# Kernel optimization log

Hardware: AMD Instinct MI355X
Metric: run time of the kernel (lower is better)

The kernel has to match this reference:

```python
import jax, jax.numpy as jnp
import numpy as np

B, N, D, H, NCB, TOPK = 4, 2048, 256, 2048, 256, 16
DP = D // 4
SCALE = float(np.sqrt(DP))
THRESH = 0.7
EPS = 1e-8


def setup_inputs() -> dict:
    key = jax.random.key(0)
    ks = jax.random.split(key, 12)
    g = lambda i, shape, s=1.0: jax.random.normal(ks[i], shape, jnp.float32) * s
    return {
        "agent_states": g(0, (B, N, D)),
        "agent_actions": g(1, (B, N, D)),
        "episodic_mem": g(2, (B, N, H)),
        "Wq": g(3, (D, DP), 0.05), "bq": jnp.zeros((DP,), jnp.float32),
        "Wk": g(4, (D, DP), 0.05), "bk": jnp.zeros((DP,), jnp.float32),
        "log_temp": jnp.asarray(0.0, jnp.float32),
        "Wc": g(5, (D, DP), 0.05), "bc": jnp.zeros((DP,), jnp.float32),
        "temp_coal": jnp.asarray(10.0, jnp.float32),
        "W_to_hdc": g(6, (D, H), 0.05), "b_to_hdc": jnp.zeros((H,), jnp.float32),
        "W_from_hdc": g(7, (H, D), 0.02), "b_from_hdc": jnp.zeros((D,), jnp.float32),
        "agent_keys": jnp.sign(g(8, (N, H))),
        "position_codes": jnp.sign(g(9, (NCB, H))),
        "step": 3,
    }


def _cosine(a, b):
    # torch F.cosine_similarity semantics, dim=-1, eps=1e-8
    na = jnp.maximum(jnp.linalg.norm(a, axis=-1), EPS)
    nb = jnp.maximum(jnp.linalg.norm(b, axis=-1), EPS)
    return jnp.sum(a * b, axis=-1) / (na * nb)


def _to_hdc_ste(x):
    soft = jnp.tanh(x * 3.0)
    hard = jnp.sign(x)
    hard = jnp.where(hard == 0, jnp.ones_like(hard), hard)
    return soft + jax.lax.stop_gradient(hard - soft)


def reference(agent_states, agent_actions, episodic_mem, Wq, bq, Wk, bk,
              log_temp, Wc, bc, temp_coal, W_to_hdc, b_to_hdc,
              W_from_hdc, b_from_hdc, agent_keys, position_codes, step):
    # ---- DynamicGraph.compute_graph: top-k dynamic attention adjacency ----
    Q = agent_actions @ Wq + bq                      # (B,N,DP)
    K = agent_actions @ Wk + bk                      # (B,N,DP)
    temp = jnp.clip(jnp.exp(log_temp), 0.1, 10.0)
    scores = jnp.einsum('bnd,bmd->bnm', Q, K) / (SCALE * temp)   # (B,N,N)
    _, topk_idx = jax.lax.top_k(scores, TOPK)                     # (B,N,k)
    bI = jnp.arange(B)[:, None, None]
    nI = jnp.arange(N)[None, :, None]
    mask = jnp.zeros_like(scores).at[bI, nI, topk_idx].set(1.0)   # scatter, like torch scatter_
    scores = scores * mask + (1.0 - mask) * -1e9
    adjacency = jax.nn.softmax(scores, axis=-1)
    # message passing over dynamic graph
    incoming = jnp.einsum('bnm,bmd->bnd', adjacency, agent_states)

    # ---- AgentCombination: sigmoid-normalized coalition mixing ----
    proj = agent_actions @ Wc + bc                   # (B,N,DP)
    pn = proj / jnp.maximum(jnp.linalg.norm(proj, axis=-1, keepdims=True), 1e-12)
    sim = jnp.einsum('bnd,bmd->bnm', pn, pn)
    cw = jax.nn.sigmoid((sim - THRESH) * temp_coal)
    cw = cw / (jnp.sum(cw, axis=-1, keepdims=True) + EPS)
    combined = jnp.einsum('bnm,bmd->bnd', cw, incoming)
    mixed = 0.8 * incoming + 0.2 * combined          # (B,N,D)

    # ---- HDCMemory: bind / write / read with STE ----
    q = _to_hdc_ste(mixed @ W_to_hdc + b_to_hdc)     # (B,N,H) bipolar via STE
    pq = q * agent_keys[None]                        # bind with agent key
    mem = jax.lax.stop_gradient(episodic_mem)        # memory read is detached in original
    pos_code = position_codes[step % NCB]            # (H,)
    new_mem = 0.95 * mem + 0.05 * (q * pos_code)     # write: bind + decay bundle
    strength = jax.nn.sigmoid(_cosine(new_mem, pq))[..., None]   # read similarity
    recall = (new_mem @ W_from_hdc + b_from_hdc) * strength      # (B,N,D)
    return mixed + recall
```

## Files before the change

kernel.cpp:

```cpp
#include <hip/hip_runtime.h>
#include <math.h>

#define BATCH 4
#define NN 2048
#define DD 256
#define HH 2048
#define DP 64
#define KTOP 16

typedef float f32x4 __attribute__((ext_vector_type(4)));
typedef short short8 __attribute__((ext_vector_type(8)));
typedef short short4v __attribute__((ext_vector_type(4)));

__device__ __forceinline__ short f2bf(float x) {
    union { float f; unsigned u; } v; v.f = x;
    unsigned r = v.u + 0x7FFFu + ((v.u >> 16) & 1u);
    return (short)(r >> 16);
}
__device__ __forceinline__ float bf2f(short s) {
    union { unsigned u; float f; } v; v.u = ((unsigned)(unsigned short)s) << 16;
    return v.f;
}

__global__ __launch_bounds__(256) void head_kernel(
    const float* __restrict__ act,
    const float* __restrict__ Wq, const float* __restrict__ bq,
    const float* __restrict__ Wk, const float* __restrict__ bk,
    const float* __restrict__ Wc, const float* __restrict__ bc,
    const float* __restrict__ W2h, const float* __restrict__ Wfh,
    float* __restrict__ Qo, float* __restrict__ Ko, short* __restrict__ Pno,
    short* __restrict__ W2hT_hi, short* __restrict__ W2hT_lo,
    short* __restrict__ WfhT_hi, short* __restrict__ WfhT_lo)
{
    __shared__ float smem[16 * 256];

    if (blockIdx.x < 512) {
        float (*rowbuf)[256] = (float(*)[256])smem;
        const int row0 = blockIdx.x * 16;
        const int t = threadIdx.x;
        const int wave = t >> 6, lane = t & 63;
        const float* src = act + (size_t)row0 * DD;
        for (int i = t; i < 16 * DD; i += 256) rowbuf[i >> 8][i & 255] = src[i];
        __syncthreads();

        float q[4], k[4], c[4];
        #pragma unroll
        for (int r = 0; r < 4; ++r) { q[r] = bq[lane]; k[r] = bk[lane]; c[r] = bc[lane]; }

        for (int d = 0; d < DD; ++d) {
            float wq = Wq[d * DP + lane];
            float wk = Wk[d * DP + lane];
            float wc = Wc[d * DP + lane];
            #pragma unroll
            for (int r = 0; r < 4; ++r) {
                float av = rowbuf[wave * 4 + r][d];
                q[r] = fmaf(av, wq, q[r]);
                k[r] = fmaf(av, wk, k[r]);
                c[r] = fmaf(av, wc, c[r]);
            }
        }
        #pragma unroll
        for (int r = 0; r < 4; ++r) {
            float ss = c[r] * c[r];
            #pragma unroll
            for (int off = 32; off; off >>= 1) ss += __shfl_xor(ss, off);
            float nrm = fmaxf(sqrtf(ss), 1e-12f);
            size_t o = (size_t)(row0 + wave * 4 + r) * DP + lane;
            Qo[o] = q[r];
            Ko[o] = k[r];
            Pno[o] = f2bf(c[r] / nrm);
        }
    } else {
        float (*tile)[33] = (float(*)[33])smem;
        int b = blockIdx.x - 512;
        const float* src; short *dhi, *dlo; int R, C, r0, c0;
        if (b < 512) {
            src = W2h; dhi = W2hT_hi; dlo = W2hT_lo; R = 256; C = 2048;
            r0 = (b >> 6) * 32; c0 = (b & 63) * 32;
        } else {
            b -= 512;
            src = Wfh; dhi = WfhT_hi; dlo = WfhT_lo; R = 2048; C = 256;
            r0 = (b >> 3) * 32; c0 = (b & 7) * 32;
        }
        int tx = threadIdx.x & 31, ty = threadIdx.x >> 5;
        #pragma unroll
        for (int i = 0; i < 4; ++i)
            tile[ty + 8 * i][tx] = src[(size_t)(r0 + ty + 8 * i) * C + c0 + tx];
        __syncthreads();
        #pragma unroll
        for (int i = 0; i < 4; ++i) {
            float v = tile[tx][ty + 8 * i];
            short hi = f2bf(v);
            size_t o = (size_t)(c0 + ty + 8 * i) * R + r0 + tx;
            dhi[o] = hi;
            dlo[o] = f2bf(v - bf2f(hi));
        }
    }
}

__global__ __launch_bounds__(512, 4) void attn_fused_kernel(
    const float* __restrict__ Q, const float* __restrict__ K,
    const float* __restrict__ log_temp,
    const float* __restrict__ states, float* __restrict__ incoming)
{
    const int t = threadIdx.x;
    const int w = t >> 6, l = t & 63;
    const int row = blockIdx.x * 8 + w;
    const int b = row >> 11;

    __shared__ float Ksh[128][68];

    const float temp = fminf(fmaxf(expf(log_temp[0]), 0.1f), 10.0f);
    const float scale = 1.0f / (8.0f * temp);

    const float* Kb = K + (size_t)b * NN * DP;
    const float4* qr4 = (const float4*)(Q + (size_t)row * DP);

    float sc[32];

    for (int ch = 0; ch < 16; ++ch) {
        __syncthreads();
        {
            int r = t >> 2, seg = t & 3;
            const float4* src = (const float4*)(Kb + (size_t)(ch * 128 + r) * DP + seg * 16);
            float4* dst = (float4*)&Ksh[r][seg * 16];
            dst[0] = src[0]; dst[1] = src[1]; dst[2] = src[2]; dst[3] = src[3];
        }
        __syncthreads();
        float a0 = 0.f, a1 = 0.f;
        const float4* k0 = (const float4*)&Ksh[l][0];
        const float4* k1 = (const float4*)&Ksh[64 + l][0];
        #pragma unroll
        for (int h = 0; h < 2; ++h) {
            float4 q[8];
            #pragma unroll
            for (int i = 0; i < 8; ++i) q[i] = qr4[h * 8 + i];
            #pragma unroll
            for (int i = 0; i < 8; ++i) {
                float4 kv0 = k0[h * 8 + i];
                float4 kv1 = k1[h * 8 + i];
                a0 = fmaf(kv0.x, q[i].x, fmaf(kv0.y, q[i].y, fmaf(kv0.z, q[i].z, fmaf(kv0.w, q[i].w, a0))));
                a1 = fmaf(kv1.x, q[i].x, fmaf(kv1.y, q[i].y, fmaf(kv1.z, q[i].z, fmaf(kv1.w, q[i].w, a1))));
            }
        }
        sc[ch * 2]     = a0 * scale;
        sc[ch * 2 + 1] = a1 * scale;
    }

    float wv = 0.f; int wm = 0;
    for (int it = 0; it < KTOP; ++it) {
        float bv = sc[0]; int bs = 0;
        #pragma unroll
        for (int i = 1; i < 32; ++i) {
            bool g = sc[i] > bv;
            bv = g ? sc[i] : bv;
            bs = g ? i : bs;
        }
        int bm = (bs >> 1) * 128 + (bs & 1) * 64 + l;
        #pragma unroll
        for (int off = 1; off < 64; off <<= 1) {
            float ov = __shfl_xor(bv, off);
            int   om = __shfl_xor(bm, off);
            bool take = (ov > bv) || (ov == bv && om < bm);
            bv = take ? ov : bv;
            bm = take ? om : bm;
        }
        if (l == it) { wv = bv; wm = bm; }
        if ((bm & 63) == l) {
            int s = ((bm >> 7) << 1) | ((bm >> 6) & 1);
            #pragma unroll
            for (int i = 0; i < 32; ++i) if (s == i) sc[i] = -3.0e38f;
        }
    }

    float mx = __shfl(wv, 0);
    float e = (l < KTOP) ? expf(wv - mx) : 0.f;
    float Z = e;
    #pragma unroll
    for (int off = 1; off < 64; off <<= 1) Z += __shfl_xor(Z, off);
    float wnorm = e / Z;

    const float* Sb = states + (size_t)b * NN * DD;
    f32x4 acc = (f32x4){0.f, 0.f, 0.f, 0.f};
    #pragma unroll
    for (int kk = 0; kk < KTOP; ++kk) {
        float wk = __shfl(wnorm, kk);
        int   ik = __shfl(wm, kk);
        const float4 v = *(const float4*)(Sb + (size_t)ik * DD + l * 4);
        acc[0] = fmaf(wk, v.x, acc[0]);
        acc[1] = fmaf(wk, v.y, acc[1]);
        acc[2] = fmaf(wk, v.z, acc[2]);
        acc[3] = fmaf(wk, v.w, acc[3]);
    }
    *(float4*)(incoming + (size_t)row * DD + l * 4) = *(float4*)&acc;
}

__global__ __launch_bounds__(256) void coal_kernel(
    const short* __restrict__ pnb_g, const float* __restrict__ incoming,
    const float* __restrict__ temp_coal, float* __restrict__ mixed)
{
    const int b  = blockIdx.x >> 7;
    const int rem = blockIdx.x & 127;
    const int n0 = (rem >> 1) * 32;
    const int dh = rem & 1;
    const int t = threadIdx.x;
    const int w = t >> 6;
    const int l = t & 63;

    __shared__ alignas(16) short pnA[32][72];
    __shared__ alignas(16) short pnB[64][72];
    __shared__ alignas(16) short cwt[32][72];
    __shared__ alignas(16) short incT[128][72];
    __shared__ float rowsum[32];

    const size_t bbase = (size_t)b * NN;

    {
        int r = t >> 3, k8 = (t & 7) * 8;
        *(short8*)&pnA[r][k8] = *(const short8*)(pnb_g + (bbase + n0 + r) * DP + k8);
    }
    if (t < 32) rowsum[t] = 0.0f;

    const float tc = temp_coal[0];

    f32x4 acc[2][2];
    #pragma unroll
    for (int i = 0; i < 2; ++i)
        #pragma unroll
        for (int j = 0; j < 2; ++j)
            acc[i][j] = (f32x4){0.f, 0.f, 0.f, 0.f};

    const int lrow = l & 15;
    const int lk   = (l >> 4) * 8;

    for (int ch = 0; ch < 32; ++ch) {
        const int m0 = ch * 64;
        __syncthreads();

        {
            int r = t >> 2, kq = (t & 3) * 16;
            const short* src = pnb_g + (bbase + m0 + r) * DP + kq;
            *(short8*)&pnB[r][kq]     = *(const short8*)src;
            *(short8*)&pnB[r][kq + 8] = *(const short8*)(src + 8);
        }
        {
            #pragma unroll
            for (int rep = 0; rep < 2; ++rep) {
                int id = t + rep * 256;
                int mq = id & 15;
                int dq = id >> 4;
                const float* incb = incoming + (bbase + m0 + mq * 4) * DD + dh * 128 + dq * 4;
                short4v col0, col1, col2, col3;
                #pragma unroll
                for (int mm = 0; mm < 4; ++mm) {
                    float4 v = *(const float4*)(incb + (size_t)mm * DD);
                    col0[mm] = f2bf(v.x);
                    col1[mm] = f2bf(v.y);
                    col2[mm] = f2bf(v.z);
                    col3[mm] = f2bf(v.w);
                }
                *(short4v*)&incT[dq * 4 + 0][mq * 4] = col0;
                *(short4v*)&incT[dq * 4 + 1][mq * 4] = col1;
                *(short4v*)&incT[dq * 4 + 2][mq * 4] = col2;
                *(short4v*)&incT[dq * 4 + 3][mq * 4] = col3;
            }
        }
        __syncthreads();

        f32x4 sacc[2];
        sacc[0] = (f32x4){0.f, 0.f, 0.f, 0.f};
        sacc[1] = (f32x4){0.f, 0.f, 0.f, 0.f};
        #pragma unroll
        for (int ks = 0; ks < 2; ++ks) {
            short8 bfr = *(const short8*)&pnB[w * 16 + lrow][lk + ks * 32];
            short8 a0  = *(const short8*)&pnA[lrow][lk + ks * 32];
            short8 a1  = *(const short8*)&pnA[16 + lrow][lk + ks * 32];
            sacc[0] = __builtin_amdgcn_mfma_f32_16x16x32_bf16(a0, bfr, sacc[0], 0, 0, 0);
            sacc[1] = __builtin_amdgcn_mfma_f32_16x16x32_bf16(a1, bfr, sacc[1], 0, 0, 0);
        }
        #pragma unroll
        for (int rt = 0; rt < 2; ++rt) {
            #pragma unroll
            for (int j = 0; j < 4; ++j) {
                int rr = rt * 16 + (l >> 4) * 4 + j;
                int cc = w * 16 + lrow;
                float cv = 1.0f / (1.0f + expf(-(sacc[rt][j] - 0.7f) * tc));
                cwt[rr][cc] = f2bf(cv);
            }
        }
        __syncthreads();

        {
            int r = t >> 3, c8 = (t & 7) * 8;
            short8 cv = *(const short8*)&cwt[r][c8];
            float p = 0.f;
            #pragma unroll
            for (int j = 0; j < 8; ++j) p += bf2f(cv[j]);
            p += __shfl_xor(p, 1);
            p += __shfl_xor(p, 2);
            p += __shfl_xor(p, 4);
            if ((t & 7) == 0) rowsum[r] += p;
        }

        #pragma unroll
        for (int ks = 0; ks < 2; ++ks) {
            short8 a0 = *(const short8*)&cwt[lrow][lk + ks * 32];
            short8 a1 = *(const short8*)&cwt[16 + lrow][lk + ks * 32];
            #pragma unroll
            for (int ct = 0; ct < 2; ++ct) {
                short8 bfr = *(const short8*)&incT[w * 32 + ct * 16 + lrow][lk + ks * 32];
                acc[0][ct] = __builtin_amdgcn_mfma_f32_16x16x32_bf16(a0, bfr, acc[0][ct], 0, 0, 0);
                acc[1][ct] = __builtin_amdgcn_mfma_f32_16x16x32_bf16(a1, bfr, acc[1][ct], 0, 0, 0);
            }
        }
    }
    __syncthreads();

    #pragma unroll
    for (int rt = 0; rt < 2; ++rt) {
        #pragma unroll
        for (int ct = 0; ct < 2; ++ct) {
            #pragma unroll
            for (int j = 0; j < 4; ++j) {
                int rr = rt * 16 + (l >> 4) * 4 + j;
                int cc = w * 32 + ct * 16 + lrow;
                float inv = 1.0f / (rowsum[rr] + 1e-8f);
                float comb = acc[rt][ct][j] * inv;
                size_t gi = (bbase + n0 + rr) * DD + dh * 128 + cc;
                mixed[gi] = 0.8f * incoming[gi] + 0.2f * comb;
            }
        }
    }
}

__global__ __launch_bounds__(256) void hdcA_kernel(
    const float* __restrict__ mixed,
    const short* __restrict__ W2hT_hi, const short* __restrict__ W2hT_lo,
    const float* __restrict__ b2h,
    unsigned short* __restrict__ qbits)
{
    const int rb = blockIdx.x >> 3;
    const int hs = blockIdx.x & 7;
    const int row0 = rb * 32;
    const int hbase = hs * 256;
    const int t = threadIdx.x;
    const int w = t >> 6, l = t & 63;
    const int lr = l & 15, lg = l >> 4;

    __shared__ short Ahi[32][264], Alo[32][264];
    __shared__ short Whi[64][136], Wlo[64][136];

    #pragma unroll
    for (int i = 0; i < 8; ++i) {
        int idx = t + i * 256;
        int r = idx >> 6, c = (idx & 63) * 4;
        float4 v = *(const float4*)(mixed + (size_t)(row0 + r) * DD + c);
        short4v hi4, lo4;
        hi4[0] = f2bf(v.x); lo4[0] = f2bf(v.x - bf2f(hi4[0]));
        hi4[1] = f2bf(v.y); lo4[1] = f2bf(v.y - bf2f(hi4[1]));
        hi4[2] = f2bf(v.z); lo4[2] = f2bf(v.z - bf2f(hi4[2]));
        hi4[3] = f2bf(v.w); lo4[3] = f2bf(v.w - bf2f(hi4[3]));
        *(short4v*)&Ahi[r][c] = hi4;
        *(short4v*)&Alo[r][c] = lo4;
    }

    for (int ch = 0; ch < 4; ++ch) {
        const int h0 = hbase + ch * 64;
        f32x4 zac[2];
        zac[0] = (f32x4){0.f, 0.f, 0.f, 0.f};
        zac[1] = (f32x4){0.f, 0.f, 0.f, 0.f};
        #pragma unroll
        for (int ks = 0; ks < 2; ++ks) {
            const int k0 = ks * 128;
            __syncthreads();
            {
                int r = t >> 2, cb = (t & 3) * 32;
                const short* sh = W2hT_hi + (size_t)(h0 + r) * DD + k0 + cb;
                const short* sl = W2hT_lo + (size_t)(h0 + r) * DD + k0 + cb;
                #pragma unroll
                for (int j = 0; j < 4; ++j) {
                    *(short8*)&Whi[r][cb + j * 8] = *(const short8*)(sh + j * 8);
                    *(short8*)&Wlo[r][cb + j * 8] = *(const short8*)(sl + j * 8);
                }
            }
            __syncthreads();
            #pragma unroll
            for (int kt = 0; kt < 4; ++kt) {
                int kk = k0 + kt * 32 + lg * 8;
                int kw = kt * 32 + lg * 8;
                short8 bhi = *(const short8*)&Whi[w * 16 + lr][kw];
                short8 blo = *(const short8*)&Wlo[w * 16 + lr][kw];
                #pragma unroll
                for (int mt = 0; mt < 2; ++mt) {
                    short8 ahi = *(const short8*)&Ahi[mt * 16 + lr][kk];
                    short8 alo = *(const short8*)&Alo[mt * 16 + lr][kk];
                    zac[mt] = __builtin_amdgcn_mfma_f32_16x16x32_bf16(ahi, bhi, zac[mt], 0, 0, 0);
                    zac[mt] = __builtin_amdgcn_mfma_f32_16x16x32_bf16(ahi, blo, zac[mt], 0, 0, 0);
                    zac[mt] = __builtin_amdgcn_mfma_f32_16x16x32_bf16(alo, bhi, zac[mt], 0, 0, 0);
                }
            }
        }
        const float bv = b2h[h0 + w * 16 + lr];
        #pragma unroll
        for (int mt = 0; mt < 2; ++mt) {
            #pragma unroll
            for (int j = 0; j < 4; ++j) {
                float z = zac[mt][j] + bv;
                unsigned long long bal = __ballot(z >= 0.0f);
                if (lr == 0)
                    qbits[(size_t)(row0 + mt * 16 + lg * 4 + j) * 128 + (h0 >> 4) + w] =
                        (unsigned short)((bal >> (lg * 16)) & 0xFFFFull);
            }
        }
    }
}

__global__ __launch_bounds__(512) void hdcB_kernel(
    const float* __restrict__ mem, const unsigned short* __restrict__ qbits,
    const float* __restrict__ pos_codes, const int* __restrict__ step,
    const short* __restrict__ WfhT_hi,
    const float* __restrict__ bfh, const float* __restrict__ keys,
    const float* __restrict__ mixed, float* __restrict__ out)
{
    const int mb = blockIdx.x >> 1, nb = blockIdx.x & 1;
    const int row0 = mb * 32, d0 = nb * 128;
    const int t = threadIdx.x;
    const int w = t >> 6, l = t & 63;
    const int wm = w >> 2, wn = w & 3;
    const int lr = l & 15, lg = l >> 4;

    __shared__ short Ahi[32][72], Alo[32][72];
    __shared__ short Bhi[128][72];
    __shared__ float sred[32][2];
    __shared__ float strenL[32];

    int st = ((step[0] % 256) + 256) % 256;
    const float* pos = pos_codes + (size_t)st * HH;

    f32x4 acc[2];
    acc[0] = (f32x4){0.f, 0.f, 0.f, 0.f};
    acc[1] = (f32x4){0.f, 0.f, 0.f, 0.f};
    float pnum = 0.f, pns = 0.f;

    const int ar = t >> 4;
    const int ah = (t & 15) * 4;
    const int arow = row0 + ar;
    const size_t memb = (size_t)arow * HH;
    const size_t keyb = (size_t)(arow & (NN - 1)) * HH;

    for (int kc = 0; kc < 32; ++kc) {
        const int h0 = kc * 64;
        __syncthreads();
        {
            float4 mv = *(const float4*)(mem + memb + h0 + ah);
            float4 kv = *(const float4*)(keys + keyb + h0 + ah);
            float4 pv = *(const float4*)(pos + h0 + ah);
            unsigned bits = (unsigned)qbits[(size_t)arow * 128 + ((h0 + ah) >> 4)] >> (ah & 15);
            float mvs[4] = { mv.x, mv.y, mv.z, mv.w };
            float kvs[4] = { kv.x, kv.y, kv.z, kv.w };
            float pvs[4] = { pv.x, pv.y, pv.z, pv.w };
            short4v hi4, lo4;
            #pragma unroll
            for (int j = 0; j < 4; ++j) {
                float q = ((bits >> j) & 1u) ? 1.0f : -1.0f;
                float nmv = fmaf(0.05f * q, pvs[j], 0.95f * mvs[j]);
                pnum = fmaf(nmv, q * kvs[j], pnum);
                pns  = fmaf(nmv, nmv, pns);
                hi4[j] = f2bf(nmv);
                lo4[j] = f2bf(nmv - bf2f(hi4[j]));
            }
            *(short4v*)&Ahi[ar][ah] = hi4;
            *(short4v*)&Alo[ar][ah] = lo4;
        }
        {
            int r = t >> 2, hb = (t & 3) * 16;
            const short* sh = WfhT_hi + (size_t)(d0 + r) * HH + h0 + hb;
            *(short8*)&Bhi[r][hb]     = *(const short8*)sh;
            *(short8*)&Bhi[r][hb + 8] = *(const short8*)(sh + 8);
        }
        __syncthreads();
        #pragma unroll
        for (int kt = 0; kt < 2; ++kt) {
            const int kk = kt * 32 + lg * 8;
            short8 ahi = *(const short8*)&Ahi[wm * 16 + lr][kk];
            short8 alo = *(const short8*)&Alo[wm * 16 + lr][kk];
            #pragma unroll
            for (int nt = 0; nt < 2; ++nt) {
                short8 bhi = *(const short8*)&Bhi[wn * 32 + nt * 16 + lr][kk];
                acc[nt] = __builtin_amdgcn_mfma_f32_16x16x32_bf16(ahi, bhi, acc[nt], 0, 0, 0);
                acc[nt] = __builtin_amdgcn_mfma_f32_16x16x32_bf16(alo, bhi, acc[nt], 0, 0, 0);
            }
        }
    }

    #pragma unroll
    for (int off = 1; off < 16; off <<= 1) {
        pnum += __shfl_xor(pnum, off);
        pns  += __shfl_xor(pns, off);
    }
    if ((t & 15) == 0) { sred[ar][0] = pnum; sred[ar][1] = pns; }
    __syncthreads();
    if (t < 32) {
        float cosv = sred[t][0] / (fmaxf(sqrtf(sred[t][1]), 1e-8f) * sqrtf(2048.0f));
        strenL[t] = 1.0f / (1.0f + expf(-cosv));
    }
    __syncthreads();

    #pragma unroll
    for (int nt = 0; nt < 2; ++nt) {
        #pragma unroll
        for (int j = 0; j < 4; ++j) {
            int rloc = wm * 16 + lg * 4 + j;
            int col = d0 + wn * 32 + nt * 16 + lr;
            size_t gi = (size_t)(row0 + rloc) * DD + col;
            out[gi] = mixed[gi] + (acc[nt][j] + bfh[col]) * strenL[rloc];
        }
    }
}

extern "C" void kernel_launch(void* const* d_in, const int* in_sizes, int n_in,
                              void* d_out, int out_size, void* d_ws, size_t ws_size,
                              hipStream_t stream) {
    const float* states    = (const float*)d_in[0];
    const float* actions   = (const float*)d_in[1];
    const float* mem       = (const float*)d_in[2];
    const float* Wq        = (const float*)d_in[3];
    const float* bq        = (const float*)d_in[4];
    const float* Wk        = (const float*)d_in[5];
    const float* bk        = (const float*)d_in[6];
    const float* log_temp  = (const float*)d_in[7];
    const float* Wc        = (const float*)d_in[8];
    const float* bc        = (const float*)d_in[9];
    const float* temp_coal = (const float*)d_in[10];
    const float* W2h       = (const float*)d_in[11];
    const float* b2h       = (const float*)d_in[12];
    const float* Wfh       = (const float*)d_in[13];
    const float* bfh       = (const float*)d_in[14];
    const float* keys      = (const float*)d_in[15];
    const float* pos_codes = (const float*)d_in[16];
    const int*   step      = (const int*)d_in[17];
    float* out = (float*)d_out;

    float* ws = (float*)d_ws;
    float* mixed    = ws;
    short* W2hT_hi  = (short*)(mixed + 2097152);
    short* W2hT_lo  = W2hT_hi + 524288;
    short* WfhT_hi  = W2hT_lo + 524288;
    short* WfhT_lo  = WfhT_hi + 524288;
    unsigned short* qbits = (unsigned short*)(WfhT_lo + 524288);
    float* Q        = (float*)(qbits + 1048576);
    float* K        = Q + 524288;
    float* incoming = K + 524288;
    short* pn_bf    = (short*)(incoming + 2097152);

    head_kernel<<<1536, 256, 0, stream>>>(actions, Wq, bq, Wk, bk, Wc, bc, W2h, Wfh,
                                          Q, K, pn_bf, W2hT_hi, W2hT_lo, WfhT_hi, WfhT_lo);
    attn_fused_kernel<<<BATCH * NN / 8, 512, 0, stream>>>(Q, K, log_temp, states, incoming);
    coal_kernel<<<BATCH * (NN / 32) * 2, 256, 0, stream>>>(pn_bf, incoming, temp_coal, mixed);
    hdcA_kernel<<<(BATCH * NN / 32) * 8, 256, 0, stream>>>(mixed, W2hT_hi, W2hT_lo, b2h, qbits);
    hdcB_kernel<<<(BATCH * NN / 32) * 2, 512, 0, stream>>>(mem, qbits, pos_codes, step,
                                                           WfhT_hi, bfh, keys, mixed, out);
}
```

Baseline: 332.0 us.

## Drop low-part weight split in HDC projection and merge coal_kernel column halves

Removes the bf16 lo-part of the transposed weight matrices, so hdcA runs two MFMA passes per tile instead of three and loads half as much weight data. head_kernel no longer writes the lo buffers. coal_kernel now covers all 256 output columns in one 512-thread block instead of two blocks per row tile, so the similarity/sigmoid matrix is computed once rather than twice. The cost is lower precision in the sign-thresholded HDC projection, which can flip signs near zero, and idle waves during the similarity phase.

```diff
diff --git a/kernel.cpp b/kernel.cpp
--- a/kernel.cpp
+++ b/kernel.cpp
@@ -29,8 +29,7 @@
     const float* __restrict__ Wc, const float* __restrict__ bc,
     const float* __restrict__ W2h, const float* __restrict__ Wfh,
     float* __restrict__ Qo, float* __restrict__ Ko, short* __restrict__ Pno,
-    short* __restrict__ W2hT_hi, short* __restrict__ W2hT_lo,
-    short* __restrict__ WfhT_hi, short* __restrict__ WfhT_lo)
+    short* __restrict__ W2hT_hi, short* __restrict__ WfhT_hi)
 {
     __shared__ float smem[16 * 256];
 
@@ -73,13 +72,13 @@
     } else {
         float (*tile)[33] = (float(*)[33])smem;
         int b = blockIdx.x - 512;
-        const float* src; short *dhi, *dlo; int R, C, r0, c0;
+        const float* src; short* dhi; int R, C, r0, c0;
         if (b < 512) {
-            src = W2h; dhi = W2hT_hi; dlo = W2hT_lo; R = 256; C = 2048;
+            src = W2h; dhi = W2hT_hi; R = 256; C = 2048;
             r0 = (b >> 6) * 32; c0 = (b & 63) * 32;
         } else {
             b -= 512;
-            src = Wfh; dhi = WfhT_hi; dlo = WfhT_lo; R = 2048; C = 256;
+            src = Wfh; dhi = WfhT_hi; R = 2048; C = 256;
             r0 = (b >> 3) * 32; c0 = (b & 7) * 32;
         }
         int tx = threadIdx.x & 31, ty = threadIdx.x >> 5;
@@ -90,10 +89,8 @@
         #pragma unroll
         for (int i = 0; i < 4; ++i) {
             float v = tile[tx][ty + 8 * i];
-            short hi = f2bf(v);
             size_t o = (size_t)(c0 + ty + 8 * i) * R + r0 + tx;
-            dhi[o] = hi;
-            dlo[o] = f2bf(v - bf2f(hi));
+            dhi[o] = f2bf(v);
         }
     }
 }
@@ -195,14 +192,12 @@
     *(float4*)(incoming + (size_t)row * DD + l * 4) = *(float4*)&acc;
 }
 
-__global__ __launch_bounds__(256) void coal_kernel(
+__global__ __launch_bounds__(512) void coal_kernel(
     const short* __restrict__ pnb_g, const float* __restrict__ incoming,
     const float* __restrict__ temp_coal, float* __restrict__ mixed)
 {
-    const int b  = blockIdx.x >> 7;
-    const int rem = blockIdx.x & 127;
-    const int n0 = (rem >> 1) * 32;
-    const int dh = rem & 1;
+    const int b  = blockIdx.x >> 6;
+    const int n0 = (blockIdx.x & 63) * 32;
     const int t = threadIdx.x;
     const int w = t >> 6;
     const int l = t & 63;
@@ -210,12 +205,12 @@
     __shared__ alignas(16) short pnA[32][72];
     __shared__ alignas(16) short pnB[64][72];
     __shared__ alignas(16) short cwt[32][72];
-    __shared__ alignas(16) short incT[128][72];
+    __shared__ alignas(16) short incT[256][72];
     __shared__ float rowsum[32];
 
     const size_t bbase = (size_t)b * NN;
 
-    {
+    if (t < 256) {
         int r = t >> 3, k8 = (t & 7) * 8;
         *(short8*)&pnA[r][k8] = *(const short8*)(pnb_g + (bbase + n0 + r) * DP + k8);
     }
@@ -238,18 +233,16 @@
         __syncthreads();
 
         {
-            int r = t >> 2, kq = (t & 3) * 16;
-            const short* src = pnb_g + (bbase + m0 + r) * DP + kq;
-            *(short8*)&pnB[r][kq]     = *(const short8*)src;
-            *(short8*)&pnB[r][kq + 8] = *(const short8*)(src + 8);
+            int r = t >> 3, k8 = (t & 7) * 8;
+            *(short8*)&pnB[r][k8] = *(const short8*)(pnb_g + (bbase + m0 + r) * DP + k8);
         }
         {
             #pragma unroll
             for (int rep = 0; rep < 2; ++rep) {
-                int id = t + rep * 256;
+                int id = t + rep * 512;
                 int mq = id & 15;
                 int dq = id >> 4;
-                const float* incb = incoming + (bbase + m0 + mq * 4) * DD + dh * 128 + dq * 4;
+                const float* incb = incoming + (bbase + m0 + mq * 4) * DD + dq * 4;
                 short4v col0, col1, col2, col3;
                 #pragma unroll
                 for (int mm = 0; mm < 4; ++mm) {
@@ -267,30 +260,32 @@
         }
         __syncthreads();
 
-        f32x4 sacc[2];
-        sacc[0] = (f32x4){0.f, 0.f, 0.f, 0.f};
-        sacc[1] = (f32x4){0.f, 0.f, 0.f, 0.f};
-        #pragma unroll
-        for (int ks = 0; ks < 2; ++ks) {
-            short8 bfr = *(const short8*)&pnB[w * 16 + lrow][lk + ks * 32];
-            short8 a0  = *(const short8*)&pnA[lrow][lk + ks * 32];
-            short8 a1  = *(const short8*)&pnA[16 + lrow][lk + ks * 32];
-            sacc[0] = __builtin_amdgcn_mfma_f32_16x16x32_bf16(a0, bfr, sacc[0], 0, 0, 0);
-            sacc[1] = __builtin_amdgcn_mfma_f32_16x16x32_bf16(a1, bfr, sacc[1], 0, 0, 0);
-        }
-        #pragma unroll
-        for (int rt = 0; rt < 2; ++rt) {
-            #pragma unroll
-            for (int j = 0; j < 4; ++j) {
-                int rr = rt * 16 + (l >> 4) * 4 + j;
-                int cc = w * 16 + lrow;
-                float cv = 1.0f / (1.0f + expf(-(sacc[rt][j] - 0.7f) * tc));
-                cwt[rr][cc] = f2bf(cv);
-            }
-        }
-        __syncthreads();
-
-        {
+        if (w < 4) {
+            f32x4 sacc[2];
+            sacc[0] = (f32x4){0.f, 0.f, 0.f, 0.f};
+            sacc[1] = (f32x4){0.f, 0.f, 0.f, 0.f};
+            #pragma unroll
+            for (int ks = 0; ks < 2; ++ks) {
+                short8 bfr = *(const short8*)&pnB[w * 16 + lrow][lk + ks * 32];
+                short8 a0  = *(const short8*)&pnA[lrow][lk + ks * 32];
+                short8 a1  = *(const short8*)&pnA[16 + lrow][lk + ks * 32];
+                sacc[0] = __builtin_amdgcn_mfma_f32_16x16x32_bf16(a0, bfr, sacc[0], 0, 0, 0);
+                sacc[1] = __builtin_amdgcn_mfma_f32_16x16x32_bf16(a1, bfr, sacc[1], 0, 0, 0);
+            }
+            #pragma unroll
+            for (int rt = 0; rt < 2; ++rt) {
+                #pragma unroll
+                for (int j = 0; j < 4; ++j) {
+                    int rr = rt * 16 + (l >> 4) * 4 + j;
+                    int cc = w * 16 + lrow;
+                    float cv = 1.0f / (1.0f + expf(-(sacc[rt][j] - 0.7f) * tc));
+                    cwt[rr][cc] = f2bf(cv);
+                }
+            }
+        }
+        __syncthreads();
+
+        if (t < 256) {
             int r = t >> 3, c8 = (t & 7) * 8;
             short8 cv = *(const short8*)&cwt[r][c8];
             float p = 0.f;
@@ -326,7 +321,7 @@
                 int cc = w * 32 + ct * 16 + lrow;
                 float inv = 1.0f / (rowsum[rr] + 1e-8f);
                 float comb = acc[rt][ct][j] * inv;
-                size_t gi = (bbase + n0 + rr) * DD + dh * 128 + cc;
+                size_t gi = (bbase + n0 + rr) * DD + cc;
                 mixed[gi] = 0.8f * incoming[gi] + 0.2f * comb;
             }
         }
@@ -335,7 +330,7 @@
 
 __global__ __launch_bounds__(256) void hdcA_kernel(
     const float* __restrict__ mixed,
-    const short* __restrict__ W2hT_hi, const short* __restrict__ W2hT_lo,
+    const short* __restrict__ W2hT_hi,
     const float* __restrict__ b2h,
     unsigned short* __restrict__ qbits)
 {
@@ -348,7 +343,7 @@
     const int lr = l & 15, lg = l >> 4;
 
     __shared__ short Ahi[32][264], Alo[32][264];
-    __shared__ short Whi[64][136], Wlo[64][136];
+    __shared__ short Whi[64][136];
 
     #pragma unroll
     for (int i = 0; i < 8; ++i) {
@@ -376,12 +371,9 @@
             {
                 int r = t >> 2, cb = (t & 3) * 32;
                 const short* sh = W2hT_hi + (size_t)(h0 + r) * DD + k0 + cb;
-                const short* sl = W2hT_lo + (size_t)(h0 + r) * DD + k0 + cb;
                 #pragma unroll
-                for (int j = 0; j < 4; ++j) {
+                for (int j = 0; j < 4; ++j)
                     *(short8*)&Whi[r][cb + j * 8] = *(const short8*)(sh + j * 8);
-                    *(short8*)&Wlo[r][cb + j * 8] = *(const short8*)(sl + j * 8);
-                }
             }
             __syncthreads();
             #pragma unroll
@@ -389,13 +381,11 @@
                 int kk = k0 + kt * 32 + lg * 8;
                 int kw = kt * 32 + lg * 8;
                 short8 bhi = *(const short8*)&Whi[w * 16 + lr][kw];
-                short8 blo = *(const short8*)&Wlo[w * 16 + lr][kw];
                 #pragma unroll
                 for (int mt = 0; mt < 2; ++mt) {
                     short8 ahi = *(const short8*)&Ahi[mt * 16 + lr][kk];
                     short8 alo = *(const short8*)&Alo[mt * 16 + lr][kk];
                     zac[mt] = __builtin_amdgcn_mfma_f32_16x16x32_bf16(ahi, bhi, zac[mt], 0, 0, 0);
-                    zac[mt] = __builtin_amdgcn_mfma_f32_16x16x32_bf16(ahi, blo, zac[mt], 0, 0, 0);
                     zac[mt] = __builtin_amdgcn_mfma_f32_16x16x32_bf16(alo, bhi, zac[mt], 0, 0, 0);
                 }
             }
@@ -544,20 +534,18 @@
     float* ws = (float*)d_ws;
     float* mixed    = ws;
     short* W2hT_hi  = (short*)(mixed + 2097152);
-    short* W2hT_lo  = W2hT_hi + 524288;
-    short* WfhT_hi  = W2hT_lo + 524288;
-    short* WfhT_lo  = WfhT_hi + 524288;
-    unsigned short* qbits = (unsigned short*)(WfhT_lo + 524288);
+    short* WfhT_hi  = W2hT_hi + 524288;
+    unsigned short* qbits = (unsigned short*)(WfhT_hi + 524288);
     float* Q        = (float*)(qbits + 1048576);
     float* K        = Q + 524288;
     float* incoming = K + 524288;
     short* pn_bf    = (short*)(incoming + 2097152);
 
     head_kernel<<<1536, 256, 0, stream>>>(actions, Wq, bq, Wk, bk, Wc, bc, W2h, Wfh,
-                                          Q, K, pn_bf, W2hT_hi, W2hT_lo, WfhT_hi, WfhT_lo);
+                                          Q, K, pn_bf, W2hT_hi, WfhT_hi);
     attn_fused_kernel<<<BATCH * NN / 8, 512, 0, stream>>>(Q, K, log_temp, states, incoming);
-    coal_kernel<<<BATCH * (NN / 32) * 2, 256, 0, stream>>>(pn_bf, incoming, temp_coal, mixed);
-    hdcA_kernel<<<(BATCH * NN / 32) * 8, 256, 0, stream>>>(mixed, W2hT_hi, W2hT_lo, b2h, qbits);
+    coal_kernel<<<BATCH * (NN / 32), 512, 0, stream>>>(pn_bf, incoming, temp_coal, mixed);
+    hdcA_kernel<<<(BATCH * NN / 32) * 8, 256, 0, stream>>>(mixed, W2hT_hi, b2h, qbits);
     hdcB_kernel<<<(BATCH * NN / 32) * 2, 512, 0, stream>>>(mem, qbits, pos_codes, step,
                                                            WfhT_hi, bfh, keys, mixed, out);
 }
```

New measurement: 327.0 us. Within noise of the previous version (-1.5%).
